# Optimization experiments

Hardware: AMD Instinct MI355X
Metric: run time of the kernel (lower is better)

## Reference

```python
import jax, jax.numpy as jnp
import numpy as np

B, T, H, L = 64, 2048, 256, 16


def setup_inputs() -> dict:
    key = jax.random.key(0)
    ks = jax.random.split(key, 6)
    x = jax.random.normal(ks[0], (B, T, H), dtype=jnp.float32)
    tags = jax.random.randint(ks[1], (B, T), 0, L).astype(jnp.int32)
    mask = jnp.ones((B, T), dtype=bool)  # torchcrf requires mask[:,0] all on
    W = jax.random.normal(ks[2], (L, H), dtype=jnp.float32) * (1.0 / np.sqrt(H))
    b = jnp.zeros((L,), dtype=jnp.float32)
    # torchcrf initializes transitions ~ U(-0.1, 0.1)
    start_transitions = jax.random.uniform(ks[3], (L,), minval=-0.1, maxval=0.1)
    end_transitions = jax.random.uniform(ks[4], (L,), minval=-0.1, maxval=0.1)
    transitions = jax.random.uniform(ks[5], (L, L), minval=-0.1, maxval=0.1)
    return {"x": x, "W": W, "b": b,
            "start_transitions": start_transitions,
            "end_transitions": end_transitions,
            "transitions": transitions,
            "tags": tags, "mask": mask}


def reference(x, W, b, start_transitions, end_transitions, transitions, tags, mask):
    # Emitter: Linear(hidden_dim -> num_labels)
    emissions = jnp.einsum('bth,lh->btl', x, W) + b  # [B,T,L]
    maskf = mask.astype(emissions.dtype)             # [B,T]

    # ---- numerator: score of the gold tag path (vectorized, no scan) ----
    emit_gold = jnp.take_along_axis(emissions, tags[..., None].astype(jnp.int32), axis=2)[..., 0]  # [B,T]
    first_tags = tags[:, 0]
    score = start_transitions[first_tags] + emit_gold[:, 0]
    trans_gold = transitions[tags[:, :-1], tags[:, 1:]]  # [B,T-1]
    score = score + jnp.sum((trans_gold + emit_gold[:, 1:]) * maskf[:, 1:], axis=1)
    seq_ends = jnp.sum(mask.astype(jnp.int32), axis=1) - 1  # index of last valid step
    last_tags = jnp.take_along_axis(tags, seq_ends[:, None], axis=1)[:, 0]
    score = score + end_transitions[last_tags]

    # ---- denominator: forward algorithm (log partition) via lax.scan over time ----
    em_t = jnp.swapaxes(emissions, 0, 1)  # [T,B,L]
    mask_t = jnp.swapaxes(mask, 0, 1)     # [T,B]
    alpha0 = start_transitions[None, :] + em_t[0]  # [B,L]

    def step(alpha, inp):
        em, m = inp  # em: [B,L], m: [B]
        # logsumexp over previous label: alpha[b,i] + transitions[i,j] + em[b,j]
        nxt = jax.nn.logsumexp(alpha[:, :, None] + transitions[None, :, :] + em[:, None, :], axis=1)
        alpha = jnp.where(m[:, None], nxt, alpha)
        return alpha, None

    alphaT, _ = jax.lax.scan(step, alpha0, (em_t[1:], mask_t[1:]))
    denom = jax.nn.logsumexp(alphaT + end_transitions[None, :], axis=1)  # [B]

    llh = score - denom          # log-likelihood per sequence
    return -jnp.mean(llh)        # reduction='mean', nll = -crf(...)
```

## Files before the change

kernel.cpp:

```cpp
#include <hip/hip_runtime.h>
#include <math.h>


#define Bb 64
#define Tt 2048
#define Hh 256
#define Ll 16
#define CHUNK 32
#define NC (Tt / CHUNK)
#define ROWS 128
#define TSTR 20

typedef __attribute__((ext_vector_type(8))) short short8;
typedef __attribute__((ext_vector_type(4))) float f32x4;

__device__ __forceinline__ unsigned pk2bf(float a, float b) {
  unsigned ua = __float_as_uint(a) + 0x8000u;
  unsigned ub = __float_as_uint(b) + 0x8000u;
  return (ua >> 16) | (ub & 0xFFFF0000u);
}
__device__ __forceinline__ short8 pack8(float4 lo, float4 hi) {
  union { int4 i; short8 s; } u;
  u.i.x = pk2bf(lo.x, lo.y);
  u.i.y = pk2bf(lo.z, lo.w);
  u.i.z = pk2bf(hi.x, hi.y);
  u.i.w = pk2bf(hi.z, hi.w);
  return u.s;
}

__global__ __launch_bounds__(256) void k_fused(const float* __restrict__ x,
                                               const float* __restrict__ W,
                                               const float* __restrict__ bias,
                                               const float* __restrict__ strans,
                                               const float* __restrict__ etrans,
                                               const float* __restrict__ trans,
                                               const int* __restrict__ tags,
                                               float* __restrict__ em0,
                                               float* __restrict__ Pout,
                                               float* __restrict__ lscale,
                                               float* __restrict__ score) {
  __shared__ float tile[ROWS * TSTR];
  __shared__ unsigned short ghb[ROWS * 16];
  __shared__ float Pbuf[4][16 * TSTR];

  const int tid = threadIdx.x, w = tid >> 6, lane = tid & 63;
  const int n = lane & 15, quad = lane >> 4;
  const int b = blockIdx.x >> 4, blk = blockIdx.x & 15;
  const int gc = blk * 4 + w;

  {
    const float4* wp4 = (const float4*)(W + (size_t)n * Hh) + quad * 2;
    short8 Bf[8];
#pragma unroll
    for (int ks = 0; ks < 8; ++ks) Bf[ks] = pack8(wp4[ks * 8], wp4[ks * 8 + 1]);
    float bs = bias[n];
    size_t Grow = (size_t)blockIdx.x * ROWS + w * 32 + n;
    const float4* xa = (const float4*)(x + Grow * Hh) + quad * 2;
    const float4* xb = (const float4*)(x + (Grow + 16) * Hh) + quad * 2;
    f32x4 acc0 = {0.f, 0.f, 0.f, 0.f}, acc1 = {0.f, 0.f, 0.f, 0.f};
#pragma unroll
    for (int ks = 0; ks < 8; ++ks) {
      short8 a0 = pack8(xa[ks * 8], xa[ks * 8 + 1]);
      short8 a1 = pack8(xb[ks * 8], xb[ks * 8 + 1]);
      acc0 = __builtin_amdgcn_mfma_f32_16x16x32_bf16(a0, Bf[ks], acc0, 0, 0, 0);
      acc1 = __builtin_amdgcn_mfma_f32_16x16x32_bf16(a1, Bf[ks], acc1, 0, 0, 0);
    }
#pragma unroll
    for (int r = 0; r < 4; ++r) {
      tile[(w * 32 + quad * 4 + r) * TSTR + n] = acc0[r] + bs;
      tile[(w * 32 + 16 + quad * 4 + r) * TSTR + n] = acc1[r] + bs;
    }
    if (blk == 0 && w == 0 && quad == 0) em0[b * 16 + n] = acc0[0] + bs;
  }
  __syncthreads();

  {
    float s2 = 0.f;
    if (lane < 32) {
      int rl = w * 32 + lane;
      int t = blk * ROWS + rl;
      int gt = b * Tt + t;
      int tag = tags[gt];
      float ev = tile[rl * TSTR + tag];
      if (t == 0) s2 = strans[tag] + ev;
      else        s2 = trans[tags[gt - 1] * 16 + tag] + ev;
      if (t == Tt - 1) s2 += etrans[tag];
    }
#pragma unroll
    for (int msk = 1; msk < 64; msk <<= 1) s2 += __shfl_xor(s2, msk);
    if (lane == 0) atomicAdd(score + b, s2);
  }

  float offsum = 0.f;
  {
    if (lane < 32) {
      int rl = w * 32 + lane;
      const float4* tp = (const float4*)(tile + rl * TSTR);
      float4 a0 = tp[0], a1 = tp[1], a2 = tp[2], a3 = tp[3];
      float m = fmaxf(fmaxf(fmaxf(fmaxf(a0.x, a0.y), fmaxf(a0.z, a0.w)),
                            fmaxf(fmaxf(a1.x, a1.y), fmaxf(a1.z, a1.w))),
                      fmaxf(fmaxf(fmaxf(a2.x, a2.y), fmaxf(a2.z, a2.w)),
                            fmaxf(fmaxf(a3.x, a3.y), fmaxf(a3.z, a3.w))));
      float4 e0 = make_float4(expf(a0.x - m), expf(a0.y - m), expf(a0.z - m), expf(a0.w - m));
      float4 e1 = make_float4(expf(a1.x - m), expf(a1.y - m), expf(a1.z - m), expf(a1.w - m));
      float4 e2 = make_float4(expf(a2.x - m), expf(a2.y - m), expf(a2.z - m), expf(a2.w - m));
      float4 e3 = make_float4(expf(a3.x - m), expf(a3.y - m), expf(a3.z - m), expf(a3.w - m));
      int4 lo, hi;
      lo.x = pk2bf(e0.x, e0.y); lo.y = pk2bf(e0.z, e0.w);
      lo.z = pk2bf(e1.x, e1.y); lo.w = pk2bf(e1.z, e1.w);
      hi.x = pk2bf(e2.x, e2.y); hi.y = pk2bf(e2.z, e2.w);
      hi.z = pk2bf(e3.x, e3.y); hi.w = pk2bf(e3.z, e3.w);
      ((int4*)ghb)[rl * 2] = lo;
      ((int4*)ghb)[rl * 2 + 1] = hi;
      int t = blk * ROWS + rl;
      offsum = (t >= 1) ? m : 0.f;
    }
#pragma unroll
    for (int msk = 1; msk < 64; msk <<= 1) offsum += __shfl_xor(offsum, msk);
  }
  __syncthreads();

  {
    short8 Eb = {0, 0, 0, 0, 0, 0, 0, 0};
    if (quad < 2) {
      float e[8];
#pragma unroll
      for (int j = 0; j < 8; ++j) e[j] = expf(trans[(quad * 8 + j) * 16 + n]);
      Eb = pack8(make_float4(e[0], e[1], e[2], e[3]), make_float4(e[4], e[5], e[6], e[7]));
    }
    short8 Aid = {0, 0, 0, 0, 0, 0, 0, 0};
    if (quad < 2 && (n >> 3) == quad) ((short*)&Aid)[n & 7] = (short)0x3F80;

    float* Pw = Pbuf[w];
    float off = offsum;
    const int sbeg = (gc == 0) ? 1 : 0;
    const unsigned short* grow = ghb + (w * 32) * 16 + n;
    short8 A = Aid;
    for (int s = sbeg; s < CHUNK; ++s) {
      f32x4 z = {0.f, 0.f, 0.f, 0.f};
      f32x4 d = __builtin_amdgcn_mfma_f32_16x16x32_bf16(A, Eb, z, 0, 0, 0);
      float g = __uint_as_float(((unsigned)grow[s * 16]) << 16);
      d[0] *= g; d[1] *= g; d[2] *= g; d[3] *= g;
      if (((s & 7) == 7) || (s == CHUNK - 1)) {
        float mx = fmaxf(fmaxf(d[0], d[1]), fmaxf(d[2], d[3]));
#pragma unroll
        for (int msk = 1; msk < 64; msk <<= 1) mx = fmaxf(mx, __shfl_xor(mx, msk));
        float inv = __builtin_amdgcn_rcpf(mx);
        d[0] *= inv; d[1] *= inv; d[2] *= inv; d[3] *= inv;
        off += logf(mx);
      }
#pragma unroll
      for (int r = 0; r < 4; ++r) Pw[(quad * 4 + r) * TSTR + n] = d[r];
      if (quad < 2) {
        const float4* pr = (const float4*)(Pw + n * TSTR + quad * 8);
        A = pack8(pr[0], pr[1]);
      }
    }
    {
      int i = lane >> 2, jg = lane & 3;
      float4 pv = *(const float4*)(Pw + i * TSTR + jg * 4);
      ((float4*)(Pout + ((size_t)(b * NC + gc)) * 256))[lane] = pv;
      if (lane == 0) lscale[b * NC + gc] = off;
    }
  }
}

__global__ __launch_bounds__(256) void k_combine(const float* __restrict__ em0,
                                                 const float* __restrict__ P,
                                                 const float* __restrict__ lscale,
                                                 const float* __restrict__ strans,
                                                 const float* __restrict__ etrans,
                                                 float* __restrict__ denom) {
  int b = blockIdx.x, tid = threadIdx.x;
  __shared__ float Pl[NC * 256];
  const float4* src = (const float4*)(P + (size_t)b * NC * 256);
  float4* dst = (float4*)Pl;
  for (int idx = tid; idx < NC * 64; idx += 256) dst[idx] = src[idx];
  __syncthreads();
  if (tid >= 64) return;
  int lane = tid;
  float ls = lscale[b * NC + lane];
#pragma unroll
  for (int m = 1; m < 64; m <<= 1) ls += __shfl_xor(ls, m);

  int j = lane & 15, ig = lane >> 4;
  float a = strans[j] + em0[b * 16 + j];
  float m0 = a;
#pragma unroll
  for (int m = 1; m < 16; m <<= 1) m0 = fmaxf(m0, __shfl_xor(m0, m));
  float v = expf(a - m0);
  float o = m0 + ls;

  for (int cc = 0; cc < NC; ++cc) {
    const float* Pc = Pl + cc * 256;
    float part = 0.f;
#pragma unroll
    for (int r = 0; r < 4; ++r) {
      int srcl = (ig << 4) + ig * 4 + r;
      float vr = __shfl(v, srcl);
      part = fmaf(vr, Pc[(ig * 4 + r) * 16 + j], part);
    }
    part += __shfl_xor(part, 16);
    part += __shfl_xor(part, 32);
    if ((cc & 3) == 3) {
      float mx = part;
#pragma unroll
      for (int m = 1; m < 16; m <<= 1) mx = fmaxf(mx, __shfl_xor(mx, m));
      o += logf(mx);
      v = part * __builtin_amdgcn_rcpf(mx);
    } else {
      v = part;
    }
  }
  float sj = v * expf(etrans[j]);
#pragma unroll
  for (int m = 1; m < 16; m <<= 1) sj += __shfl_xor(sj, m);
  if (lane == 0) denom[b] = o + logf(sj);
}

__global__ __launch_bounds__(64) void k_final(const float* __restrict__ score,
                                              const float* __restrict__ denom,
                                              float* __restrict__ out) {
  int lane = threadIdx.x;
  float llh = score[lane] - denom[lane];
#pragma unroll
  for (int m = 1; m < 64; m <<= 1) llh += __shfl_xor(llh, m);
  if (lane == 0) out[0] = -llh * (1.0f / 64.0f);
}

extern "C" void kernel_launch(void* const* d_in, const int* in_sizes, int n_in,
                              void* d_out, int out_size, void* d_ws, size_t ws_size,
                              hipStream_t stream) {
  const float* x = (const float*)d_in[0];
  const float* W = (const float*)d_in[1];
  const float* bias = (const float*)d_in[2];
  const float* strans = (const float*)d_in[3];
  const float* etrans = (const float*)d_in[4];
  const float* trans = (const float*)d_in[5];
  const int* tags = (const int*)d_in[6];

  float* ws = (float*)d_ws;
  float* em0 = ws;
  float* P = em0 + Bb * 16;
  float* lscale = P + (size_t)Bb * NC * 256;
  float* score = lscale + Bb * NC;
  float* denom = score + Bb;
  float* out = (float*)d_out;

  hipMemsetAsync(score, 0, Bb * sizeof(float), stream);
  hipLaunchKernelGGL(k_fused, dim3(Bb * Tt / ROWS), dim3(256), 0, stream,
                     x, W, bias, strans, etrans, trans, tags, em0, P, lscale, score);
  hipLaunchKernelGGL(k_combine, dim3(Bb), dim3(256), 0, stream, em0, P, lscale, strans, etrans, denom);
  hipLaunchKernelGGL(k_final, dim3(1), dim3(64), 0, stream, score, denom, out);
}
```

Measured before the change: 243.1 us.

## Replace sequential chunk matrix chain with parallel tree reduction of transfer matrices

Each wavefront used to build its chunk's 16x16 transfer product through 32 dependent MFMA steps with LDS round-trips. It now forms a per-step transfer matrix for each pair of time steps, then multiplies them pairwise in a log-depth tree, moving operands between layouts with register shuffles instead of LDS. Fixed power-of-two scale factors plus occasional renormalisation keep the bf16 values in range, and a constant log offset corrects the result. The per-step emission exponentials are now kept in fp32, and two block barriers are dropped because each wave only reads its own rows. The aim is to cut the serial dependency latency, at the cost of more MFMAs and shuffles, plus some precision risk from the fixed scaling.

```diff
diff --git a/kernel.cpp b/kernel.cpp
--- a/kernel.cpp
+++ b/kernel.cpp
@@ -10,6 +10,7 @@
 #define NC (Tt / CHUNK)
 #define ROWS 128
 #define TSTR 20
+#define GSTR 20
 
 typedef __attribute__((ext_vector_type(8))) short short8;
 typedef __attribute__((ext_vector_type(4))) float f32x4;
@@ -26,6 +27,25 @@
   u.i.z = pk2bf(hi.x, hi.y);
   u.i.w = pk2bf(hi.z, hi.w);
   return u.s;
+}
+
+__device__ __forceinline__ short8 convCF(f32x4 d, float sc, int n, int q) {
+  float scq = (q < 2) ? sc : 0.f;
+  int l0 = (n + 32 * q) & 63, l1 = (l0 + 16) & 63;
+  float v0 = __shfl(d[0], l0) * scq, v1 = __shfl(d[1], l0) * scq;
+  float v2 = __shfl(d[2], l0) * scq, v3 = __shfl(d[3], l0) * scq;
+  float v4 = __shfl(d[0], l1) * scq, v5 = __shfl(d[1], l1) * scq;
+  float v6 = __shfl(d[2], l1) * scq, v7 = __shfl(d[3], l1) * scq;
+  return pack8(make_float4(v0, v1, v2, v3), make_float4(v4, v5, v6, v7));
+}
+
+__device__ __forceinline__ void renorm(f32x4& d, float& off) {
+  float mx = fmaxf(fmaxf(d[0], d[1]), fmaxf(d[2], d[3]));
+#pragma unroll
+  for (int msk = 1; msk < 64; msk <<= 1) mx = fmaxf(mx, __shfl_xor(mx, msk));
+  float inv = __builtin_amdgcn_rcpf(mx);
+  d[0] *= inv; d[1] *= inv; d[2] *= inv; d[3] *= inv;
+  off += logf(mx);
 }
 
 __global__ __launch_bounds__(256) void k_fused(const float* __restrict__ x,
@@ -40,7 +60,7 @@
                                                float* __restrict__ lscale,
                                                float* __restrict__ score) {
   __shared__ float tile[ROWS * TSTR];
-  __shared__ unsigned short ghb[ROWS * 16];
+  __shared__ float ghf[ROWS * GSTR];
   __shared__ float Pbuf[4][16 * TSTR];
 
   const int tid = threadIdx.x, w = tid >> 6, lane = tid & 63;
@@ -72,7 +92,6 @@
     }
     if (blk == 0 && w == 0 && quad == 0) em0[b * 16 + n] = acc0[0] + bs;
   }
-  __syncthreads();
 
   {
     float s2 = 0.f;
@@ -101,67 +120,84 @@
                             fmaxf(fmaxf(a1.x, a1.y), fmaxf(a1.z, a1.w))),
                       fmaxf(fmaxf(fmaxf(a2.x, a2.y), fmaxf(a2.z, a2.w)),
                             fmaxf(fmaxf(a3.x, a3.y), fmaxf(a3.z, a3.w))));
-      float4 e0 = make_float4(expf(a0.x - m), expf(a0.y - m), expf(a0.z - m), expf(a0.w - m));
-      float4 e1 = make_float4(expf(a1.x - m), expf(a1.y - m), expf(a1.z - m), expf(a1.w - m));
-      float4 e2 = make_float4(expf(a2.x - m), expf(a2.y - m), expf(a2.z - m), expf(a2.w - m));
-      float4 e3 = make_float4(expf(a3.x - m), expf(a3.y - m), expf(a3.z - m), expf(a3.w - m));
-      int4 lo, hi;
-      lo.x = pk2bf(e0.x, e0.y); lo.y = pk2bf(e0.z, e0.w);
-      lo.z = pk2bf(e1.x, e1.y); lo.w = pk2bf(e1.z, e1.w);
-      hi.x = pk2bf(e2.x, e2.y); hi.y = pk2bf(e2.z, e2.w);
-      hi.z = pk2bf(e3.x, e3.y); hi.w = pk2bf(e3.z, e3.w);
-      ((int4*)ghb)[rl * 2] = lo;
-      ((int4*)ghb)[rl * 2 + 1] = hi;
+      float4* gp = (float4*)(ghf + rl * GSTR);
+      gp[0] = make_float4(expf(a0.x - m), expf(a0.y - m), expf(a0.z - m), expf(a0.w - m));
+      gp[1] = make_float4(expf(a1.x - m), expf(a1.y - m), expf(a1.z - m), expf(a1.w - m));
+      gp[2] = make_float4(expf(a2.x - m), expf(a2.y - m), expf(a2.z - m), expf(a2.w - m));
+      gp[3] = make_float4(expf(a3.x - m), expf(a3.y - m), expf(a3.z - m), expf(a3.w - m));
       int t = blk * ROWS + rl;
       offsum = (t >= 1) ? m : 0.f;
     }
 #pragma unroll
     for (int msk = 1; msk < 64; msk <<= 1) offsum += __shfl_xor(offsum, msk);
   }
-  __syncthreads();
-
-  {
-    short8 Eb = {0, 0, 0, 0, 0, 0, 0, 0};
-    if (quad < 2) {
-      float e[8];
-#pragma unroll
-      for (int j = 0; j < 8; ++j) e[j] = expf(trans[(quad * 8 + j) * 16 + n]);
-      Eb = pack8(make_float4(e[0], e[1], e[2], e[3]), make_float4(e[4], e[5], e[6], e[7]));
-    }
-    short8 Aid = {0, 0, 0, 0, 0, 0, 0, 0};
-    if (quad < 2 && (n >> 3) == quad) ((short*)&Aid)[n & 7] = (short)0x3F80;
-
+
+  {
+    float Ecol[8], Erow[8];
+#pragma unroll
+    for (int j = 0; j < 8; ++j) {
+      Ecol[j] = (quad < 2) ? expf(trans[(quad * 8 + j) * 16 + n]) : 0.f;
+      Erow[j] = (quad < 2) ? expf(trans[n * 16 + quad * 8 + j]) : 0.f;
+    }
+    const float* gw = ghf + (w * 32) * GSTR;
+    float off = offsum + 112.0f * 0.6931471805599453f;
+    f32x4 z = {0.f, 0.f, 0.f, 0.f};
+    const short8 zf = {0, 0, 0, 0, 0, 0, 0, 0};
+
+    short8 cur[16];
+#pragma unroll
+    for (int i = 0; i < 16; ++i) {
+      short8 fL = zf;
+      if (gc == 0 && i == 0) {
+        if (quad < 2 && (n >> 3) == quad) ((short*)&fL)[n & 7] = (short)0x3F80;
+      } else if (quad < 2) {
+        const float* gp = gw + (2 * i) * GSTR + quad * 8;
+        float4 ga = *(const float4*)gp;
+        float4 gb = *(const float4*)(gp + 4);
+        fL = pack8(make_float4(Erow[0] * ga.x, Erow[1] * ga.y, Erow[2] * ga.z, Erow[3] * ga.w),
+                   make_float4(Erow[4] * gb.x, Erow[5] * gb.y, Erow[6] * gb.z, Erow[7] * gb.w));
+      }
+      short8 fR = zf;
+      if (quad < 2) {
+        float g = gw[(2 * i + 1) * GSTR + n];
+        fR = pack8(make_float4(Ecol[0] * g, Ecol[1] * g, Ecol[2] * g, Ecol[3] * g),
+                   make_float4(Ecol[4] * g, Ecol[5] * g, Ecol[6] * g, Ecol[7] * g));
+      }
+      f32x4 d = ((i & 1) == 0) ? __builtin_amdgcn_mfma_f32_16x16x32_bf16(fR, fL, z, 0, 0, 0)
+                               : __builtin_amdgcn_mfma_f32_16x16x32_bf16(fL, fR, z, 0, 0, 0);
+      cur[i] = convCF(d, 0.03125f, n, quad);
+    }
+#pragma unroll
+    for (int i = 0; i < 8; ++i) {
+      f32x4 d = ((i & 1) == 0)
+                    ? __builtin_amdgcn_mfma_f32_16x16x32_bf16(cur[2 * i + 1], cur[2 * i], z, 0, 0, 0)
+                    : __builtin_amdgcn_mfma_f32_16x16x32_bf16(cur[2 * i], cur[2 * i + 1], z, 0, 0, 0);
+      cur[i] = convCF(d, 0.125f, n, quad);
+    }
+#pragma unroll
+    for (int i = 0; i < 4; ++i) {
+      f32x4 d = ((i & 1) == 0)
+                    ? __builtin_amdgcn_mfma_f32_16x16x32_bf16(cur[2 * i + 1], cur[2 * i], z, 0, 0, 0)
+                    : __builtin_amdgcn_mfma_f32_16x16x32_bf16(cur[2 * i], cur[2 * i + 1], z, 0, 0, 0);
+      renorm(d, off);
+      cur[i] = convCF(d, 1.0f, n, quad);
+    }
+#pragma unroll
+    for (int i = 0; i < 2; ++i) {
+      f32x4 d = ((i & 1) == 0)
+                    ? __builtin_amdgcn_mfma_f32_16x16x32_bf16(cur[2 * i + 1], cur[2 * i], z, 0, 0, 0)
+                    : __builtin_amdgcn_mfma_f32_16x16x32_bf16(cur[2 * i], cur[2 * i + 1], z, 0, 0, 0);
+      cur[i] = convCF(d, 0.0625f, n, quad);
+    }
+    f32x4 d = __builtin_amdgcn_mfma_f32_16x16x32_bf16(cur[0], cur[1], z, 0, 0, 0);
+    renorm(d, off);
     float* Pw = Pbuf[w];
-    float off = offsum;
-    const int sbeg = (gc == 0) ? 1 : 0;
-    const unsigned short* grow = ghb + (w * 32) * 16 + n;
-    short8 A = Aid;
-    for (int s = sbeg; s < CHUNK; ++s) {
-      f32x4 z = {0.f, 0.f, 0.f, 0.f};
-      f32x4 d = __builtin_amdgcn_mfma_f32_16x16x32_bf16(A, Eb, z, 0, 0, 0);
-      float g = __uint_as_float(((unsigned)grow[s * 16]) << 16);
-      d[0] *= g; d[1] *= g; d[2] *= g; d[3] *= g;
-      if (((s & 7) == 7) || (s == CHUNK - 1)) {
-        float mx = fmaxf(fmaxf(d[0], d[1]), fmaxf(d[2], d[3]));
-#pragma unroll
-        for (int msk = 1; msk < 64; msk <<= 1) mx = fmaxf(mx, __shfl_xor(mx, msk));
-        float inv = __builtin_amdgcn_rcpf(mx);
-        d[0] *= inv; d[1] *= inv; d[2] *= inv; d[3] *= inv;
-        off += logf(mx);
-      }
-#pragma unroll
-      for (int r = 0; r < 4; ++r) Pw[(quad * 4 + r) * TSTR + n] = d[r];
-      if (quad < 2) {
-        const float4* pr = (const float4*)(Pw + n * TSTR + quad * 8);
-        A = pack8(pr[0], pr[1]);
-      }
-    }
-    {
-      int i = lane >> 2, jg = lane & 3;
-      float4 pv = *(const float4*)(Pw + i * TSTR + jg * 4);
-      ((float4*)(Pout + ((size_t)(b * NC + gc)) * 256))[lane] = pv;
-      if (lane == 0) lscale[b * NC + gc] = off;
-    }
+#pragma unroll
+    for (int r = 0; r < 4; ++r) Pw[(quad * 4 + r) * TSTR + n] = d[r];
+    int i2 = lane >> 2, jg = lane & 3;
+    float4 pv = *(const float4*)(Pw + i2 * TSTR + jg * 4);
+    ((float4*)(Pout + ((size_t)(b * NC + gc)) * 256))[lane] = pv;
+    if (lane == 0) lscale[b * NC + gc] = off;
   }
 }
 
```

New measurement: 256.5 us. 1.06x slower.
